# Optimization experiments

Measured on AMD Instinct MI355X. Metric: run time of the kernel, lower is better.

## Reference

```python
import jax, jax.numpy as jnp
import numpy as np

N_NODES = 100000
N_EDGES = 3200000
N_GRAPHS = 4096
IN_CH = 128
HID = 128


def setup_inputs() -> dict:
    key = jax.random.key(0)
    ks = jax.random.split(key, 16)
    x = jax.random.normal(ks[0], (N_NODES, IN_CH), dtype=jnp.float32)
    edge_index = jax.random.randint(ks[1], (2, N_EDGES), 0, N_NODES, dtype=jnp.int64)
    batch = jnp.sort(jax.random.randint(ks[2], (N_NODES,), 0, N_GRAPHS, dtype=jnp.int64))
    def lin(k, fan_in, fan_out):
        bound = 1.0 / np.sqrt(fan_in)
        kw, kb = jax.random.split(k)
        W = jax.random.uniform(kw, (fan_in, fan_out), minval=-bound, maxval=bound, dtype=jnp.float32)
        b = jax.random.uniform(kb, (fan_out,), minval=-bound, maxval=bound, dtype=jnp.float32)
        return W, b
    W1, b1 = lin(ks[3], IN_CH, HID)
    W2, b2 = lin(ks[4], HID, HID)
    W3, b3 = lin(ks[5], HID, HID)
    lw1, lb1 = lin(ks[6], HID, HID // 2)
    lw2, lb2 = lin(ks[7], HID // 2, 1)
    return {"x": x, "edge_index": edge_index, "batch": batch,
            "W1": W1, "b1": b1, "W2": W2, "b2": b2, "W3": W3, "b3": b3,
            "lw1": lw1, "lb1": lb1, "lw2": lw2, "lb2": lb2}


def _gcn_conv(x, src, dst, norm, W, b, n_nodes):
    h = x @ W                              # [N, out]
    msg = h[src] * norm[:, None]           # gather + scale  [E+N, out]
    agg = jax.ops.segment_sum(msg, dst, num_segments=n_nodes)  # scatter-add
    return agg + b


def reference(x, edge_index, batch, W1, b1, W2, b2, W3, b3, lw1, lb1, lw2, lb2):
    n = x.shape[0]
    loop = jnp.arange(n, dtype=edge_index.dtype)
    src = jnp.concatenate([edge_index[0], loop])   # self-loops appended
    dst = jnp.concatenate([edge_index[1], loop])
    deg = jax.ops.segment_sum(jnp.ones_like(dst, dtype=x.dtype), dst, num_segments=n)
    dinv = deg ** -0.5                              # deg >= 1 due to self-loops
    norm = dinv[src] * dinv[dst]                    # symmetric normalization

    h = x
    for W, b in ((W1, b1), (W2, b2), (W3, b3)):
        h = jax.nn.relu(_gcn_conv(h, src, dst, norm, W, b, n))
        # dropout is identity in eval mode

    # global mean pool over graphs
    sums = jax.ops.segment_sum(h, batch, num_segments=N_GRAPHS)
    counts = jax.ops.segment_sum(jnp.ones((n,), dtype=h.dtype), batch, num_segments=N_GRAPHS)
    pooled = sums / jnp.maximum(counts, 1.0)[:, None]   # [G, HID]

    out = jax.nn.relu(pooled @ lw1 + lb1)
    out = out @ lw2 + lb2
    return out[:, 0]
```

## Files before the change

kernel.cpp:

```cpp
#include <hip/hip_runtime.h>


constexpr int HID = 128;
constexpr int BIN_SHIFT = 8;
constexpr int MAXBINS = 512;

typedef float f32x4 __attribute__((ext_vector_type(4)));
typedef short short8 __attribute__((ext_vector_type(8)));

static __device__ __forceinline__ unsigned bf16rne(float f) {
    unsigned u = __float_as_uint(f);
    return (u + 0x7FFFu + ((u >> 16) & 1u)) >> 16;
}
static __device__ __forceinline__ unsigned packbf16(float lo, float hi) {
    return bf16rne(lo) | (bf16rne(hi) << 16);
}
static __device__ __forceinline__ float blo(unsigned u) { return __uint_as_float(u << 16); }
static __device__ __forceinline__ float bhi(unsigned u) { return __uint_as_float(u & 0xFFFF0000u); }

__global__ __launch_bounds__(256) void k_binhist(const int* __restrict__ dst,
                                                 int* __restrict__ binc,
                                                 int nE, int nbins) {
    __shared__ int h[MAXBINS];
    const int tid = threadIdx.x;
    for (int t = tid; t < nbins; t += 256) h[t] = 0;
    __syncthreads();
    const long long e0 = (long long)blockIdx.x * 4096;
#pragma unroll
    for (int k = 0; k < 16; ++k) {
        long long e = e0 + k * 256 + tid;
        if (e < nE) atomicAdd(&h[dst[e] >> BIN_SHIFT], 1);
    }
    __syncthreads();
    for (int t = tid; t < nbins; t += 256)
        if (h[t]) atomicAdd(&binc[t], h[t]);
}

__global__ __launch_bounds__(512) void k_scanbins(const int* __restrict__ binc,
                                                  int* __restrict__ bin_start,
                                                  int* __restrict__ bin_cursor,
                                                  int nbins, int nE) {
    __shared__ int lds[512];
    const int tid = threadIdx.x;
    int v = (tid < nbins) ? binc[tid] : 0;
    lds[tid] = v;
    __syncthreads();
    for (int off = 1; off < 512; off <<= 1) {
        int u = (tid >= off) ? lds[tid - off] : 0;
        __syncthreads();
        lds[tid] += u;
        __syncthreads();
    }
    int excl = lds[tid] - v;
    if (tid < nbins) { bin_start[tid] = excl; bin_cursor[tid] = excl; }
    if (tid == 0) bin_start[nbins] = nE;
}

__global__ __launch_bounds__(256) void k_stage(const int* __restrict__ src,
                                               const int* __restrict__ dst,
                                               int* __restrict__ bin_cursor,
                                               int2* __restrict__ staged,
                                               int nE, int nbins) {
    __shared__ int hist[MAXBINS];
    __shared__ int wbase[MAXBINS];
    __shared__ int rank[MAXBINS];
    const int tid = threadIdx.x;
    const long long e0 = (long long)blockIdx.x * 4096;
    int es[16], ed[16];
#pragma unroll
    for (int k = 0; k < 16; ++k) {
        long long e = e0 + k * 256 + tid;
        if (e < nE) { es[k] = src[e]; ed[k] = dst[e]; }
        else        { es[k] = 0; ed[k] = -1; }
    }
    for (int t = tid; t < nbins; t += 256) { hist[t] = 0; rank[t] = 0; }
    __syncthreads();
#pragma unroll
    for (int k = 0; k < 16; ++k)
        if (ed[k] >= 0) atomicAdd(&hist[ed[k] >> BIN_SHIFT], 1);
    __syncthreads();
    for (int t = tid; t < nbins; t += 256)
        wbase[t] = hist[t] ? atomicAdd(&bin_cursor[t], hist[t]) : 0;
    __syncthreads();
#pragma unroll
    for (int k = 0; k < 16; ++k)
        if (ed[k] >= 0) {
            int b = ed[k] >> BIN_SHIFT;
            int r = atomicAdd(&rank[b], 1);
            staged[wbase[b] + r] = make_int2(es[k], ed[k]);
        }
}

__global__ __launch_bounds__(256) void k_place2(const int* __restrict__ bin_start,
                                                const int2* __restrict__ staged,
                                                int* __restrict__ esrc,
                                                int* __restrict__ row_start,
                                                float* __restrict__ dinv, int nN) {
    __shared__ int cnt[1 << BIN_SHIFT];
    __shared__ int sc[1 << BIN_SHIFT];
    const int b = blockIdx.x;
    const int tid = threadIdx.x;
    const int d0 = b << BIN_SHIFT;
    const int dend = min(d0 + (1 << BIN_SHIFT), nN);
    const int p0 = bin_start[b];
    const int p1 = bin_start[b + 1];
    cnt[tid] = 0;
    __syncthreads();
    for (int i = p0 + tid; i < p1; i += 256)
        atomicAdd(&cnt[staged[i].y - d0], 1);
    __syncthreads();
    const int my = cnt[tid];
    sc[tid] = my;
    __syncthreads();
    for (int off = 1; off < 256; off <<= 1) {
        int v = (tid >= off) ? sc[tid - off] : 0;
        __syncthreads();
        sc[tid] += v;
        __syncthreads();
    }
    const int excl = sc[tid] - my;
    const int d = d0 + tid;
    if (d < dend) {
        row_start[d] = p0 + excl;
        dinv[d] = rsqrtf((float)my + 1.0f);
    }
    if (tid == 0 && dend == nN) row_start[nN] = p1;
    __syncthreads();
    cnt[tid] = p0 + excl;
    __syncthreads();
    for (int i = p0 + tid; i < p1; i += 256) {
        int2 pr = staged[i];
        int pos = atomicAdd(&cnt[pr.y - d0], 1);
        esrc[pos] = pr.x;
    }
}

template <bool A_F32>
__global__ __launch_bounds__(256) void k_gemm_mfma(const void* __restrict__ Aptr,
                                                   const float* __restrict__ W,
                                                   const float* __restrict__ dinv,
                                                   unsigned* __restrict__ h16, int n) {
    __shared__ unsigned lds[128 * 68];
    const int tid  = threadIdx.x;
    const int lane = tid & 63;
    const int w    = tid >> 6;
    const int colb = lane & 15;
    const int kg   = lane >> 4;
    const int row0 = blockIdx.x * 64;

    for (int it = 0; it < 32; ++it) {
        int f = it * 256 + tid;
        int c = f & 127, k2 = f >> 7;
        float w0 = W[(size_t)(2 * k2) * HID + c];
        float w1 = W[(size_t)(2 * k2 + 1) * HID + c];
        lds[c * 68 + k2] = packbf16(w0, w1);
    }

    const int r = row0 + w * 16 + colb;
    uint4 a[4] = {};
    if (r < n) {
        if constexpr (A_F32) {
            const float* A = (const float*)Aptr;
#pragma unroll
            for (int kc = 0; kc < 4; ++kc) {
                const float* p = A + (size_t)r * HID + kc * 32 + kg * 8;
                float4 f0 = *(const float4*)(p);
                float4 f1 = *(const float4*)(p + 4);
                a[kc].x = packbf16(f0.x, f0.y);
                a[kc].y = packbf16(f0.z, f0.w);
                a[kc].z = packbf16(f1.x, f1.y);
                a[kc].w = packbf16(f1.z, f1.w);
            }
        } else {
            const unsigned* A16 = (const unsigned*)Aptr;
#pragma unroll
            for (int kc = 0; kc < 4; ++kc)
                a[kc] = *(const uint4*)(A16 + (size_t)r * 64 + kc * 16 + kg * 4);
        }
    }
    __syncthreads();

    f32x4 acc[8] = {};
#pragma unroll
    for (int ct = 0; ct < 8; ++ct) {
#pragma unroll
        for (int kc = 0; kc < 4; ++kc) {
            uint4 bu = *(const uint4*)&lds[(ct * 16 + colb) * 68 + kc * 16 + kg * 4];
            acc[ct] = __builtin_amdgcn_mfma_f32_16x16x32_bf16(
                __builtin_bit_cast(short8, a[kc]),
                __builtin_bit_cast(short8, bu),
                acc[ct], 0, 0, 0);
        }
    }

    __syncthreads();
    float* Cb = (float*)lds;
#pragma unroll
    for (int ct = 0; ct < 8; ++ct)
#pragma unroll
        for (int reg = 0; reg < 4; ++reg)
            Cb[(w * 16 + kg * 4 + reg) * 132 + ct * 16 + colb] = acc[ct][reg];
    __syncthreads();
    for (int it = 0; it < 16; ++it) {
        int f = it * 256 + tid;
        int rl = f >> 6, cw = f & 63;
        int gr = row0 + rl;
        if (gr < n) {
            float di = dinv[gr];
            float2 v = *(const float2*)&Cb[rl * 132 + 2 * cw];
            h16[(size_t)gr * 64 + cw] = packbf16(v.x * di, v.y * di);
        }
    }
}

__global__ __launch_bounds__(256) void k_agg16(const int* __restrict__ row_start,
                                               const int* __restrict__ esrc,
                                               const float* __restrict__ dinv,
                                               const unsigned* __restrict__ h16,
                                               const float* __restrict__ bias,
                                               unsigned* __restrict__ out16, int n,
                                               float* __restrict__ pool_sums,
                                               const int* __restrict__ batch) {
    int t = blockIdx.x * 256 + threadIdx.x;
    int node = t >> 6;
    if (node >= n) return;
    const int lane = t & 63;
    int e0 = row_start[node], e1 = row_start[node + 1];
    e0 = __builtin_amdgcn_readfirstlane(e0);
    e1 = __builtin_amdgcn_readfirstlane(e1);
    float dd = dinv[node];

    unsigned su = h16[(size_t)node * 64 + lane];
    float ax = blo(su), ay = bhi(su);

    int e = e0;
    for (; e + 4 <= e1; e += 4) {
        int s0 = __builtin_amdgcn_readfirstlane(esrc[e + 0]);
        int s1 = __builtin_amdgcn_readfirstlane(esrc[e + 1]);
        int s2 = __builtin_amdgcn_readfirstlane(esrc[e + 2]);
        int s3 = __builtin_amdgcn_readfirstlane(esrc[e + 3]);
        unsigned u0 = h16[(size_t)s0 * 64 + lane];
        unsigned u1 = h16[(size_t)s1 * 64 + lane];
        unsigned u2 = h16[(size_t)s2 * 64 + lane];
        unsigned u3 = h16[(size_t)s3 * 64 + lane];
        ax += blo(u0) + blo(u1) + blo(u2) + blo(u3);
        ay += bhi(u0) + bhi(u1) + bhi(u2) + bhi(u3);
    }
    for (; e < e1; ++e) {
        int s = __builtin_amdgcn_readfirstlane(esrc[e]);
        unsigned u = h16[(size_t)s * 64 + lane];
        ax += blo(u);
        ay += bhi(u);
    }

    const float2 bv = *(const float2*)(bias + 2 * lane);
    float ox = fmaxf(ax * dd + bv.x, 0.f);
    float oy = fmaxf(ay * dd + bv.y, 0.f);
    if (out16) {
        out16[(size_t)node * 64 + lane] = packbf16(ox, oy);
    } else {
        float* p = &pool_sums[(size_t)batch[node] * HID + 2 * lane];
        atomicAdd(p, ox);
        atomicAdd(p + 1, oy);
    }
}

__global__ __launch_bounds__(256) void k_count(const int* __restrict__ batch,
                                               float* __restrict__ cnt, int n) {
    int i = blockIdx.x * 256 + threadIdx.x;
    if (i < n) atomicAdd(&cnt[batch[i]], 1.0f);
}

__global__ __launch_bounds__(64) void k_mlp(const float* __restrict__ sums,
                                            const float* __restrict__ cnt,
                                            const float* __restrict__ lw1,
                                            const float* __restrict__ lb1,
                                            const float* __restrict__ lw2,
                                            const float* __restrict__ lb2,
                                            float* __restrict__ out) {
    int g = blockIdx.x;
    int j = threadIdx.x;
    float inv = 1.0f / fmaxf(cnt[g], 1.0f);
    const float* srow = sums + (size_t)g * HID;
    float acc = lb1[j];
#pragma unroll 8
    for (int k = 0; k < HID; ++k) acc += srow[k] * inv * lw1[k * 64 + j];
    acc = fmaxf(acc, 0.0f);
    float prod = acc * lw2[j];
#pragma unroll
    for (int off = 32; off > 0; off >>= 1) prod += __shfl_down(prod, off);
    if (j == 0) out[g] = prod + lb2[0];
}

extern "C" void kernel_launch(void* const* d_in, const int* in_sizes, int n_in,
                              void* d_out, int out_size, void* d_ws, size_t ws_size,
                              hipStream_t stream) {
    const float* x   = (const float*)d_in[0];
    const int*   ei  = (const int*)d_in[1];
    const int*   bat = (const int*)d_in[2];
    const float* W1  = (const float*)d_in[3];
    const float* b1  = (const float*)d_in[4];
    const float* W2  = (const float*)d_in[5];
    const float* b2  = (const float*)d_in[6];
    const float* W3  = (const float*)d_in[7];
    const float* b3  = (const float*)d_in[8];
    const float* lw1 = (const float*)d_in[9];
    const float* lb1 = (const float*)d_in[10];
    const float* lw2 = (const float*)d_in[11];
    const float* lb2 = (const float*)d_in[12];
    float* out = (float*)d_out;

    const int nN = in_sizes[2];
    const int nE = in_sizes[1] / 2;
    const int G  = out_size;
    const int* src = ei;
    const int* dst = ei + nE;

    const int nbins = (nN + (1 << BIN_SHIFT) - 1) >> BIN_SHIFT;

    char* p = (char*)d_ws;
    auto alloc = [&](size_t bytes) { char* r = p; p += (bytes + 255) & ~(size_t)255; return r; };
    unsigned* act16     = (unsigned*)alloc(sizeof(unsigned) * (size_t)nN * 64);
    unsigned* h16       = (unsigned*)alloc(sizeof(unsigned) * (size_t)nN * 64);
    float*    dinv      = (float*)alloc(sizeof(float) * nN);
    float*    sums      = (float*)alloc(sizeof(float) * (size_t)G * HID);
    float*    cnt       = (float*)alloc(sizeof(float) * G);
    int*      binc      = (int*)alloc(sizeof(int) * (nbins + 1));
    int*      bin_start = (int*)alloc(sizeof(int) * (nbins + 1));
    int*      bin_cur   = (int*)alloc(sizeof(int) * (nbins + 1));
    int*      row_start = (int*)alloc(sizeof(int) * (nN + 1));
    int*      esrc      = (int*)alloc(sizeof(int) * (size_t)nE);
    int2*     staged    = (int2*)h16;

    const int gemmGrid = (nN + 63) / 64;
    const int aggGrid  = (int)(((long long)nN * 64 + 255) / 256);
    const int edgeWGs  = (int)(((long long)nE + 4095) / 4096);

    hipMemsetAsync(binc, 0, sizeof(int) * nbins, stream);
    k_binhist<<<edgeWGs, 256, 0, stream>>>(dst, binc, nE, nbins);
    k_scanbins<<<1, 512, 0, stream>>>(binc, bin_start, bin_cur, nbins, nE);
    k_stage<<<edgeWGs, 256, 0, stream>>>(src, dst, bin_cur, staged, nE, nbins);
    k_place2<<<nbins, 256, 0, stream>>>(bin_start, staged, esrc, row_start, dinv, nN);

    hipMemsetAsync(sums, 0, sizeof(float) * ((size_t)G * HID + G), stream);
    k_count<<<(nN + 255) / 256, 256, 0, stream>>>(bat, cnt, nN);

    k_gemm_mfma<true ><<<gemmGrid, 256, 0, stream>>>(x, W1, dinv, h16, nN);
    k_agg16<<<aggGrid, 256, 0, stream>>>(row_start, esrc, dinv, h16, b1, act16, nN, nullptr, nullptr);
    k_gemm_mfma<false><<<gemmGrid, 256, 0, stream>>>(act16, W2, dinv, h16, nN);
    k_agg16<<<aggGrid, 256, 0, stream>>>(row_start, esrc, dinv, h16, b2, act16, nN, nullptr, nullptr);
    k_gemm_mfma<false><<<gemmGrid, 256, 0, stream>>>(act16, W3, dinv, h16, nN);
    k_agg16<<<aggGrid, 256, 0, stream>>>(row_start, esrc, dinv, h16, b3, nullptr, nN, sums, bat);

    k_mlp<<<G, 64, 0, stream>>>(sums, cnt, lw1, lb1, lw2, lb2, out);
}
```

Measured before the change: 533.0 us.

## Replace bin histogram+scan with fixed-capacity bins and packed 32-bit staging

```diff
diff --git a/kernel.cpp b/kernel.cpp
--- a/kernel.cpp
+++ b/kernel.cpp
@@ -4,6 +4,7 @@
 constexpr int HID = 128;
 constexpr int BIN_SHIFT = 8;
 constexpr int MAXBINS = 512;
+constexpr int CAP_SHIFT = 14;
 
 typedef float f32x4 __attribute__((ext_vector_type(4)));
 typedef short short8 __attribute__((ext_vector_type(8)));
@@ -18,48 +19,15 @@
 static __device__ __forceinline__ float blo(unsigned u) { return __uint_as_float(u << 16); }
 static __device__ __forceinline__ float bhi(unsigned u) { return __uint_as_float(u & 0xFFFF0000u); }
 
-__global__ __launch_bounds__(256) void k_binhist(const int* __restrict__ dst,
-                                                 int* __restrict__ binc,
-                                                 int nE, int nbins) {
-    __shared__ int h[MAXBINS];
-    const int tid = threadIdx.x;
-    for (int t = tid; t < nbins; t += 256) h[t] = 0;
-    __syncthreads();
-    const long long e0 = (long long)blockIdx.x * 4096;
-#pragma unroll
-    for (int k = 0; k < 16; ++k) {
-        long long e = e0 + k * 256 + tid;
-        if (e < nE) atomicAdd(&h[dst[e] >> BIN_SHIFT], 1);
-    }
-    __syncthreads();
-    for (int t = tid; t < nbins; t += 256)
-        if (h[t]) atomicAdd(&binc[t], h[t]);
-}
-
-__global__ __launch_bounds__(512) void k_scanbins(const int* __restrict__ binc,
-                                                  int* __restrict__ bin_start,
-                                                  int* __restrict__ bin_cursor,
-                                                  int nbins, int nE) {
-    __shared__ int lds[512];
-    const int tid = threadIdx.x;
-    int v = (tid < nbins) ? binc[tid] : 0;
-    lds[tid] = v;
-    __syncthreads();
-    for (int off = 1; off < 512; off <<= 1) {
-        int u = (tid >= off) ? lds[tid - off] : 0;
-        __syncthreads();
-        lds[tid] += u;
-        __syncthreads();
-    }
-    int excl = lds[tid] - v;
-    if (tid < nbins) { bin_start[tid] = excl; bin_cursor[tid] = excl; }
-    if (tid == 0) bin_start[nbins] = nE;
+__global__ __launch_bounds__(256) void k_initcur(int* __restrict__ bin_cur, int nbins) {
+    int b = blockIdx.x * 256 + threadIdx.x;
+    if (b < nbins) bin_cur[b] = b << CAP_SHIFT;
 }
 
 __global__ __launch_bounds__(256) void k_stage(const int* __restrict__ src,
                                                const int* __restrict__ dst,
                                                int* __restrict__ bin_cursor,
-                                               int2* __restrict__ staged,
+                                               unsigned* __restrict__ staged,
                                                int nE, int nbins) {
     __shared__ int hist[MAXBINS];
     __shared__ int wbase[MAXBINS];
@@ -87,14 +55,17 @@
         if (ed[k] >= 0) {
             int b = ed[k] >> BIN_SHIFT;
             int r = atomicAdd(&rank[b], 1);
-            staged[wbase[b] + r] = make_int2(es[k], ed[k]);
+            int w = wbase[b] + r;
+            if (w < ((b + 1) << CAP_SHIFT))
+                staged[w] = ((unsigned)(ed[k] & ((1 << BIN_SHIFT) - 1)) << 24) | (unsigned)es[k];
         }
 }
 
-__global__ __launch_bounds__(256) void k_place2(const int* __restrict__ bin_start,
-                                                const int2* __restrict__ staged,
+__global__ __launch_bounds__(256) void k_place2(const int* __restrict__ bin_cur,
+                                                const unsigned* __restrict__ staged,
                                                 int* __restrict__ esrc,
                                                 int* __restrict__ row_start,
+                                                int* __restrict__ row_end,
                                                 float* __restrict__ dinv, int nN) {
     __shared__ int cnt[1 << BIN_SHIFT];
     __shared__ int sc[1 << BIN_SHIFT];
@@ -102,12 +73,12 @@
     const int tid = threadIdx.x;
     const int d0 = b << BIN_SHIFT;
     const int dend = min(d0 + (1 << BIN_SHIFT), nN);
-    const int p0 = bin_start[b];
-    const int p1 = bin_start[b + 1];
+    const int p0 = b << CAP_SHIFT;
+    const int p1 = bin_cur[b];
     cnt[tid] = 0;
     __syncthreads();
     for (int i = p0 + tid; i < p1; i += 256)
-        atomicAdd(&cnt[staged[i].y - d0], 1);
+        atomicAdd(&cnt[staged[i] >> 24], 1);
     __syncthreads();
     const int my = cnt[tid];
     sc[tid] = my;
@@ -122,16 +93,16 @@
     const int d = d0 + tid;
     if (d < dend) {
         row_start[d] = p0 + excl;
+        row_end[d]   = p0 + excl + my;
         dinv[d] = rsqrtf((float)my + 1.0f);
     }
-    if (tid == 0 && dend == nN) row_start[nN] = p1;
     __syncthreads();
     cnt[tid] = p0 + excl;
     __syncthreads();
     for (int i = p0 + tid; i < p1; i += 256) {
-        int2 pr = staged[i];
-        int pos = atomicAdd(&cnt[pr.y - d0], 1);
-        esrc[pos] = pr.x;
+        unsigned pr = staged[i];
+        int pos = atomicAdd(&cnt[pr >> 24], 1);
+        esrc[pos] = (int)(pr & 0xFFFFFFu);
     }
 }
 
@@ -214,6 +185,7 @@
 }
 
 __global__ __launch_bounds__(256) void k_agg16(const int* __restrict__ row_start,
+                                               const int* __restrict__ row_end,
                                                const int* __restrict__ esrc,
                                                const float* __restrict__ dinv,
                                                const unsigned* __restrict__ h16,
@@ -225,7 +197,7 @@
     int node = t >> 6;
     if (node >= n) return;
     const int lane = t & 63;
-    int e0 = row_start[node], e1 = row_start[node + 1];
+    int e0 = row_start[node], e1 = row_end[node];
     e0 = __builtin_amdgcn_readfirstlane(e0);
     e1 = __builtin_amdgcn_readfirstlane(e1);
     float dd = dinv[node];
@@ -317,40 +289,38 @@
     const int* dst = ei + nE;
 
     const int nbins = (nN + (1 << BIN_SHIFT) - 1) >> BIN_SHIFT;
+    const size_t capTotal = (size_t)nbins << CAP_SHIFT;
 
     char* p = (char*)d_ws;
     auto alloc = [&](size_t bytes) { char* r = p; p += (bytes + 255) & ~(size_t)255; return r; };
     unsigned* act16     = (unsigned*)alloc(sizeof(unsigned) * (size_t)nN * 64);
-    unsigned* h16       = (unsigned*)alloc(sizeof(unsigned) * (size_t)nN * 64);
+    unsigned* h16       = (unsigned*)alloc(sizeof(unsigned) * ((size_t)nN * 64 > capTotal ? (size_t)nN * 64 : capTotal));
     float*    dinv      = (float*)alloc(sizeof(float) * nN);
     float*    sums      = (float*)alloc(sizeof(float) * (size_t)G * HID);
     float*    cnt       = (float*)alloc(sizeof(float) * G);
-    int*      binc      = (int*)alloc(sizeof(int) * (nbins + 1));
-    int*      bin_start = (int*)alloc(sizeof(int) * (nbins + 1));
     int*      bin_cur   = (int*)alloc(sizeof(int) * (nbins + 1));
-    int*      row_start = (int*)alloc(sizeof(int) * (nN + 1));
-    int*      esrc      = (int*)alloc(sizeof(int) * (size_t)nE);
-    int2*     staged    = (int2*)h16;
+    int*      row_start = (int*)alloc(sizeof(int) * nN);
+    int*      row_end   = (int*)alloc(sizeof(int) * nN);
+    int*      esrc      = (int*)alloc(sizeof(int) * capTotal);
+    unsigned* staged    = (unsigned*)h16;
 
     const int gemmGrid = (nN + 63) / 64;
     const int aggGrid  = (int)(((long long)nN * 64 + 255) / 256);
     const int edgeWGs  = (int)(((long long)nE + 4095) / 4096);
 
-    hipMemsetAsync(binc, 0, sizeof(int) * nbins, stream);
-    k_binhist<<<edgeWGs, 256, 0, stream>>>(dst, binc, nE, nbins);
-    k_scanbins<<<1, 512, 0, stream>>>(binc, bin_start, bin_cur, nbins, nE);
+    k_initcur<<<(nbins + 255) / 256, 256, 0, stream>>>(bin_cur, nbins);
     k_stage<<<edgeWGs, 256, 0, stream>>>(src, dst, bin_cur, staged, nE, nbins);
-    k_place2<<<nbins, 256, 0, stream>>>(bin_start, staged, esrc, row_start, dinv, nN);
+    k_place2<<<nbins, 256, 0, stream>>>(bin_cur, staged, esrc, row_start, row_end, dinv, nN);
 
     hipMemsetAsync(sums, 0, sizeof(float) * ((size_t)G * HID + G), stream);
     k_count<<<(nN + 255) / 256, 256, 0, stream>>>(bat, cnt, nN);
 
     k_gemm_mfma<true ><<<gemmGrid, 256, 0, stream>>>(x, W1, dinv, h16, nN);
-    k_agg16<<<aggGrid, 256, 0, stream>>>(row_start, esrc, dinv, h16, b1, act16, nN, nullptr, nullptr);
+    k_agg16<<<aggGrid, 256, 0, stream>>>(row_start, row_end, esrc, dinv, h16, b1, act16, nN, nullptr, nullptr);
     k_gemm_mfma<false><<<gemmGrid, 256, 0, stream>>>(act16, W2, dinv, h16, nN);
-    k_agg16<<<aggGrid, 256, 0, stream>>>(row_start, esrc, dinv, h16, b2, act16, nN, nullptr, nullptr);
+    k_agg16<<<aggGrid, 256, 0, stream>>>(row_start, row_end, esrc, dinv, h16, b2, act16, nN, nullptr, nullptr);
     k_gemm_mfma<false><<<gemmGrid, 256, 0, stream>>>(act16, W3, dinv, h16, nN);
-    k_agg16<<<aggGrid, 256, 0, stream>>>(row_start, esrc, dinv, h16, b3, nullptr, nN, sums, bat);
+    k_agg16<<<aggGrid, 256, 0, stream>>>(row_start, row_end, esrc, dinv, h16, b3, nullptr, nN, sums, bat);
 
     k_mlp<<<G, 64, 0, stream>>>(sums, cnt, lw1, lb1, lw2, lb2, out);
 }
```

Result: faster. 513.4 us (-3.7%).
